# Performance work log

Measured on AMD Instinct MI355X. Metric: run time of the kernel, lower is better.

Reference implementation:

```python
import jax, jax.numpy as jnp
import numpy as np

B, S, H = 8, 2048, 1024

def setup_inputs() -> dict:
    key = jax.random.key(0)
    k1, k2 = jax.random.split(key)
    inputs = jax.random.normal(k1, (B, S, H), dtype=jnp.float32)
    # PyTorch Linear weight [out, in]; init ~ U(-1/sqrt(H), 1/sqrt(H)) approximated with scaled normal
    W = jax.random.normal(k2, (H, H), dtype=jnp.float32) * (1.0 / np.sqrt(H))
    b = jnp.zeros((H,), dtype=jnp.float32)
    return {"inputs": inputs, "W": W, "b": b}

def reference(inputs, W, b):
    # QW = inputs @ W^T + b   (nn.Linear)
    QW = jnp.einsum('bsh,oh->bso', inputs, W) + b  # [B,S,H]
    # score = QW @ inputs^T  (no scaling, no mask)
    score = jnp.einsum('bqh,bkh->bqk', QW, inputs)  # [B,S,S]
    attn = jax.nn.softmax(score, axis=2)
    # output = attn @ inputs
    output = jnp.einsum('bqk,bkh->bqh', attn, inputs)  # [B,S,H]
    return output
```

## Files before the change

### kernel.cpp

```cpp
#include <hip/hip_runtime.h>
#include <hip/hip_bf16.h>
#include <hip/hip_fp16.h>

typedef unsigned short u16;
typedef __attribute__((ext_vector_type(8))) _Float16 f16x8;
typedef __attribute__((ext_vector_type(4))) float f32x4;

#define B_ 8
#define S_ 2048
#define H_ 1024
#define M_ (B_ * S_)

__device__ __forceinline__ u16 f2h(float f) {
  _Float16 h = (_Float16)f;
  return __builtin_bit_cast(u16, h);
}

__global__ void f32_to_f16_kernel(const float* __restrict__ x,
                                  u16* __restrict__ o, int n4) {
  int stride = gridDim.x * blockDim.x;
  for (int i = blockIdx.x * blockDim.x + threadIdx.x; i < n4; i += stride) {
    float4 v = reinterpret_cast<const float4*>(x)[i];
    ushort4 h;
    h.x = f2h(v.x); h.y = f2h(v.y); h.z = f2h(v.z); h.w = f2h(v.w);
    reinterpret_cast<ushort4*>(o)[i] = h;
  }
}

__global__ void transpose_f32_kernel(const float* __restrict__ x,
                                     u16* __restrict__ xt,
                                     u16* __restrict__ xf) {
  __shared__ u16 t[64][65];
  int b = blockIdx.z, s0 = blockIdx.x * 64, h0 = blockIdx.y * 64;
  int tx = threadIdx.x, ty = threadIdx.y;
  const float* src = x + ((size_t)b * S_ + s0) * H_ + h0;
  u16* dstf = xf + ((size_t)b * S_ + s0) * H_ + h0;
#pragma unroll
  for (int i = 0; i < 4; ++i) {
    u16 h = f2h(src[(size_t)(ty + 16 * i) * H_ + tx]);
    t[ty + 16 * i][tx] = h;
    dstf[(size_t)(ty + 16 * i) * H_ + tx] = h;
  }
  __syncthreads();
  u16* dst = xt + ((size_t)b * H_ + h0) * S_ + s0;
#pragma unroll
  for (int i = 0; i < 4; ++i)
    dst[(size_t)(ty + 16 * i) * S_ + tx] = t[tx][ty + 16 * i];
}

__device__ __forceinline__ void async_stage16(const u16* g, u16* l) {
  __builtin_amdgcn_global_load_lds(
      (__attribute__((address_space(1))) void*)g,
      (__attribute__((address_space(3))) void*)l, 16, 0, 0);
}

template <int OM>
__global__ __launch_bounds__(512) void gemm8_kernel(
    const u16* __restrict__ A, const u16* __restrict__ B,
    float* __restrict__ Cf, u16* __restrict__ Ch,
    const float* __restrict__ bias,
    int lda, int ldb, int ldc, int K,
    long sAz, long sBz, long sCz) {
  __shared__ __align__(16) u16 sA[2][256 * 64];
  __shared__ __align__(16) u16 sB[2][256 * 64];

  int gx = gridDim.x, gy = gridDim.y;
  int nwg = gx * gy * gridDim.z;
  int wgid = blockIdx.x + gx * (blockIdx.y + gy * blockIdx.z);
  int q = nwg >> 3, r = nwg & 7;
  int xcd = wgid & 7, idx = wgid >> 3;
  int nid = (xcd < r ? xcd * (q + 1) : r * (q + 1) + (xcd - r) * q) + idx;
  int bxi = nid % gx, t2 = nid / gx;
  int byi = t2 % gy, bzi = t2 / gy;

  int tid = threadIdx.x, wave = tid >> 6, lane = tid & 63;
  int wm = wave >> 2, wn = wave & 3;
  int bm = bxi * 256, bn = byi * 256;
  long zA = (long)bzi * sAz;
  long zB = (long)bzi * sBz;
  long zC = (long)bzi * sCz;
  const u16* gA = A + zA + (size_t)bm * lda;
  const u16* gB = B + zB + (size_t)bn * ldb;

  int srow = tid >> 3;
  int scolb = (tid & 7) << 4;
  int sco = (scolb ^ ((srow & 7) << 4)) >> 1;
  size_t aO0 = (size_t)srow * lda + sco, aO1 = aO0 + (size_t)64 * lda;
  size_t bO0 = (size_t)srow * ldb + sco, bO1 = bO0 + (size_t)64 * ldb;
  int ld0 = srow * 64 + (scolb >> 1), ld1 = ld0 + 64 * 64;

  auto stgA = [&](int slot, int half, int kofs) {
    const u16* g = gA + (size_t)(half * 128) * lda + kofs;
    u16* l = &sA[slot][half * 8192];
    async_stage16(g + aO0, l + ld0);
    async_stage16(g + aO1, l + ld1);
  };
  auto stgB = [&](int slot, int half, int kofs) {
    const u16* g = gB + (size_t)(half * 128) * ldb + kofs;
    u16* l = &sB[slot][half * 8192];
    async_stage16(g + bO0, l + ld0);
    async_stage16(g + bO1, l + ld1);
  };

  int la = lane & 15;
  int kg = (lane >> 4) << 4;
  auto frag = [&](const u16* base, int row, int colb) -> f16x8 {
    int off = (row << 7) + (colb ^ ((row & 7) << 4));
    return *reinterpret_cast<const f16x8*>(
        reinterpret_cast<const char*>(base) + off);
  };

  f16x8 aF[4][2], bF[2][2];
  f32x4 acc[8][4] = {};

  auto RA = [&](int slot, int qm) {
#pragma unroll
    for (int j = 0; j < 4; ++j)
#pragma unroll
      for (int ks = 0; ks < 2; ++ks)
        aF[j][ks] = frag(sA[slot], qm * 128 + (j * 2 + wm) * 16 + la,
                         ks * 64 + kg);
  };
  auto RB = [&](int slot, int qn) {
#pragma unroll
    for (int i = 0; i < 2; ++i)
#pragma unroll
      for (int ks = 0; ks < 2; ++ks)
        bF[i][ks] = frag(sB[slot], qn * 128 + (i * 4 + wn) * 16 + la,
                         ks * 64 + kg);
  };
  auto MM = [&](int qm, int qn) {
#pragma unroll
    for (int ks = 0; ks < 2; ++ks)
#pragma unroll
      for (int j = 0; j < 4; ++j)
#pragma unroll
        for (int i = 0; i < 2; ++i)
          acc[qm * 4 + j][qn * 2 + i] = __builtin_amdgcn_mfma_f32_16x16x32_f16(
              aF[j][ks], bF[i][ks], acc[qm * 4 + j][qn * 2 + i], 0, 0, 0);
  };

#define VM6 asm volatile("s_waitcnt vmcnt(6)" ::: "memory")
#define VM0 asm volatile("s_waitcnt vmcnt(0)" ::: "memory")
#define LG8 asm volatile("s_waitcnt lgkmcnt(8)" ::: "memory")
#define BAR __builtin_amdgcn_s_barrier()
#define LG0                                              \
  asm volatile("s_waitcnt lgkmcnt(0)" ::: "memory");     \
  __builtin_amdgcn_sched_barrier(0)
#define MFMA_CL(qm, qn)                 \
  __builtin_amdgcn_s_setprio(1);        \
  MM(qm, qn);                           \
  __builtin_amdgcn_s_setprio(0)

  int NT = K >> 6;
  stgA(0, 0, 0); stgB(0, 0, 0); stgB(0, 1, 0); stgA(0, 1, 0);
  if (NT > 1) { stgA(1, 0, 64); stgB(1, 1, 64); stgA(1, 1, 64); }
  VM6;
  BAR;

  for (int t = 0; t < NT; ++t) {
    int s = t & 1, ns = s ^ 1;
    int k1 = (t + 1) << 6, k2 = (t + 2) << 6;
    bool p1 = (t + 1 < NT), p2 = (t + 2 < NT);
    RA(s, 0); RB(s, 0);
    if (p1) stgB(ns, 0, k1);
    LG8;
    BAR; LG0; MFMA_CL(0, 0); BAR;
    RB(s, 1);
    if (p2) stgA(s, 0, k2);
    BAR; LG0; MFMA_CL(0, 1); BAR;
    RA(s, 1);
    if (p2) stgB(s, 1, k2);
    BAR; LG0; MFMA_CL(1, 1); BAR;
    RB(s, 0);
    if (p2) stgA(s, 1, k2);
    if (t < NT - 2) { VM6; } else if (t == NT - 2) { VM0; }
    BAR; LG0; MFMA_CL(1, 0); BAR;
  }
#undef VM6
#undef VM0
#undef LG8
#undef BAR
#undef LG0
#undef MFMA_CL

#pragma unroll
  for (int mf = 0; mf < 8; ++mf) {
    int qm = mf >> 2, j = mf & 3;
    int row = bm + qm * 128 + (j * 2 + wm) * 16 + (lane >> 4) * 4;
#pragma unroll
    for (int nf = 0; nf < 4; ++nf) {
      int qn = nf >> 1, i = nf & 1;
      int col = bn + qn * 128 + (i * 4 + wn) * 16 + la;
#pragma unroll
      for (int r = 0; r < 4; ++r) {
        float v = acc[mf][nf][r];
        if constexpr (OM == 1) {
          Ch[zC + (size_t)(row + r) * ldc + col] = f2h(v + bias[col]);
        } else {
          Cf[zC + (size_t)(row + r) * ldc + col] = v;
        }
      }
    }
  }
}

__global__ __launch_bounds__(256) void softmax_kernel(const float* __restrict__ sc,
                                                      u16* __restrict__ attn,
                                                      int opitch) {
  __shared__ float red[4];
  size_t row = blockIdx.x;
  const float* p = sc + row * S_;
  u16* o = attn + row * (size_t)opitch;
  int t = threadIdx.x;
  float4 v0 = reinterpret_cast<const float4*>(p)[t];
  float4 v1 = reinterpret_cast<const float4*>(p)[t + 256];
  float mx = fmaxf(fmaxf(fmaxf(v0.x, v0.y), fmaxf(v0.z, v0.w)),
                   fmaxf(fmaxf(v1.x, v1.y), fmaxf(v1.z, v1.w)));
#pragma unroll
  for (int d = 32; d > 0; d >>= 1) mx = fmaxf(mx, __shfl_xor(mx, d));
  if ((t & 63) == 0) red[t >> 6] = mx;
  __syncthreads();
  mx = fmaxf(fmaxf(red[0], red[1]), fmaxf(red[2], red[3]));
  float e[8];
  e[0] = __expf(v0.x - mx); e[1] = __expf(v0.y - mx);
  e[2] = __expf(v0.z - mx); e[3] = __expf(v0.w - mx);
  e[4] = __expf(v1.x - mx); e[5] = __expf(v1.y - mx);
  e[6] = __expf(v1.z - mx); e[7] = __expf(v1.w - mx);
  float s = ((e[0] + e[1]) + (e[2] + e[3])) + ((e[4] + e[5]) + (e[6] + e[7]));
#pragma unroll
  for (int d = 32; d > 0; d >>= 1) s += __shfl_xor(s, d);
  __syncthreads();
  if ((t & 63) == 0) red[t >> 6] = s;
  __syncthreads();
  s = (red[0] + red[1]) + (red[2] + red[3]);
  float inv = 1.0f / s;
  ushort4 h0, h1;
  h0.x = f2h(e[0] * inv); h0.y = f2h(e[1] * inv);
  h0.z = f2h(e[2] * inv); h0.w = f2h(e[3] * inv);
  h1.x = f2h(e[4] * inv); h1.y = f2h(e[5] * inv);
  h1.z = f2h(e[6] * inv); h1.w = f2h(e[7] * inv);
  reinterpret_cast<ushort4*>(o)[t] = h0;
  reinterpret_cast<ushort4*>(o)[t + 256] = h1;
}

extern "C" void kernel_launch(void* const* d_in, const int* in_sizes, int n_in,
                              void* d_out, int out_size, void* d_ws, size_t ws_size,
                              hipStream_t stream) {
  const float* X = (const float*)d_in[0];
  const float* W = (const float*)d_in[1];
  const float* bias = (const float*)d_in[2];
  float* out = (float*)d_out;
  char* ws = (char*)d_ws;

  const size_t MB = 1ull << 20;
  u16* XF = (u16*)(ws);
  u16* WF = (u16*)(ws + 32 * MB);
  u16* XT = (u16*)(ws + 34 * MB);
  u16* QW = (u16*)(ws + 66 * MB);
  float* SC = (float*)(ws + 98 * MB);
  u16* PF = (u16*)(ws + 162 * MB);

  int plan = (ws_size >= 226 * MB) ? 2 : (ws_size >= 163 * MB) ? 1 : 0;
  int CB = (plan >= 1) ? 4 : 2;
  int nch = B_ / CB;

  f32_to_f16_kernel<<<1024, 256, 0, stream>>>(W, WF, H_ * H_ / 4);
  transpose_f32_kernel<<<dim3(S_ / 64, H_ / 64, B_), dim3(64, 16), 0, stream>>>(
      X, XT, XF);
  gemm8_kernel<1><<<dim3(M_ / 256, H_ / 256, 1), 512, 0, stream>>>(
      XF, WF, nullptr, QW, bias, H_, H_, H_, H_, 0, 0, 0);
  for (int ch = 0; ch < nch; ++ch) {
    long off = (long)ch * CB;
    gemm8_kernel<0><<<dim3(S_ / 256, S_ / 256, CB), 512, 0, stream>>>(
        QW + off * S_ * H_, XF + off * S_ * H_, SC, nullptr, nullptr,
        H_, H_, S_, H_, (long)S_ * H_, (long)S_ * H_, (long)S_ * S_);
    if (plan == 2) {
      softmax_kernel<<<CB * S_, 256, 0, stream>>>(
          SC, PF + off * S_ * S_, S_);
    } else {
      softmax_kernel<<<CB * S_, 256, 0, stream>>>(
          SC, (u16*)SC, 2 * S_);
      gemm8_kernel<0><<<dim3(S_ / 256, H_ / 256, CB), 512, 0, stream>>>(
          (u16*)SC, XT + off * (long)H_ * S_,
          out + off * (long)S_ * H_, nullptr, nullptr,
          2 * S_, S_, H_, S_, (long)S_ * 2 * S_, (long)H_ * S_, (long)S_ * H_);
    }
  }
  if (plan == 2) {
    gemm8_kernel<0><<<dim3(S_ / 256, H_ / 256, B_), 512, 0, stream>>>(
        PF, XT, out, nullptr, nullptr,
        S_, S_, H_, S_, (long)S_ * S_, (long)H_ * S_, (long)S_ * H_);
  }
}
```

Before: 257.3 us.

## Keep both B fragment halves in registers, drop redundant barriers, vectorize transpose

The GEMM main loop now holds the B fragments for both N-halves in separate registers. The last quadrant can then reuse the B fragments loaded earlier instead of reloading them from LDS, and several of the paired barriers around each MFMA cluster are removed to cut synchronisation stalls. The transpose/convert kernel switches to float4 loads and ushort4 stores with 256 threads and a padded LDS tile, which should make global accesses wider. The gemm changes raise register pressure, and fewer barriers could expose LDS write-after-read hazards if the staging order is not actually safe.

```diff
diff --git a/kernel.cpp b/kernel.cpp
--- a/kernel.cpp
+++ b/kernel.cpp
@@ -27,25 +27,34 @@
   }
 }
 
-__global__ void transpose_f32_kernel(const float* __restrict__ x,
-                                     u16* __restrict__ xt,
-                                     u16* __restrict__ xf) {
-  __shared__ u16 t[64][65];
+__global__ __launch_bounds__(256) void transpose_f32_kernel(
+    const float* __restrict__ x, u16* __restrict__ xt, u16* __restrict__ xf) {
+  __shared__ u16 t[64][72];
   int b = blockIdx.z, s0 = blockIdx.x * 64, h0 = blockIdx.y * 64;
-  int tx = threadIdx.x, ty = threadIdx.y;
-  const float* src = x + ((size_t)b * S_ + s0) * H_ + h0;
-  u16* dstf = xf + ((size_t)b * S_ + s0) * H_ + h0;
-#pragma unroll
-  for (int i = 0; i < 4; ++i) {
-    u16 h = f2h(src[(size_t)(ty + 16 * i) * H_ + tx]);
-    t[ty + 16 * i][tx] = h;
-    dstf[(size_t)(ty + 16 * i) * H_ + tx] = h;
+  int tid = threadIdx.x;
+  int row = tid & 63, seg = tid >> 6;
+  const float* src = x + ((size_t)(b * S_ + s0 + row)) * H_ + h0 + seg * 16;
+  u16* dstf = xf + ((size_t)(b * S_ + s0 + row)) * H_ + h0 + seg * 16;
+#pragma unroll
+  for (int j = 0; j < 4; ++j) {
+    float4 v = reinterpret_cast<const float4*>(src)[j];
+    ushort4 h;
+    h.x = f2h(v.x); h.y = f2h(v.y); h.z = f2h(v.z); h.w = f2h(v.w);
+    reinterpret_cast<ushort4*>(dstf)[j] = h;
+    *reinterpret_cast<ushort4*>(&t[row][seg * 16 + j * 4]) = h;
   }
   __syncthreads();
-  u16* dst = xt + ((size_t)b * H_ + h0) * S_ + s0;
-#pragma unroll
-  for (int i = 0; i < 4; ++i)
-    dst[(size_t)(ty + 16 * i) * S_ + tx] = t[tx][ty + 16 * i];
+  int hh = tid & 63, ss = tid >> 6;
+  u16* dst = xt + ((size_t)(b * H_ + h0 + hh)) * S_ + s0 + ss * 16;
+#pragma unroll
+  for (int j = 0; j < 4; ++j) {
+    ushort4 o;
+    o.x = t[ss * 16 + j * 4 + 0][hh];
+    o.y = t[ss * 16 + j * 4 + 1][hh];
+    o.z = t[ss * 16 + j * 4 + 2][hh];
+    o.w = t[ss * 16 + j * 4 + 3][hh];
+    reinterpret_cast<ushort4*>(dst)[j] = o;
+  }
 }
 
 __device__ __forceinline__ void async_stage16(const u16* g, u16* l) {
@@ -110,7 +119,8 @@
         reinterpret_cast<const char*>(base) + off);
   };
 
-  f16x8 aF[4][2], bF[2][2];
+  f16x8 aF[4][2];
+  f16x8 bF[2][2][2];
   f32x4 acc[8][4] = {};
 
   auto RA = [&](int slot, int qm) {
@@ -126,8 +136,8 @@
     for (int i = 0; i < 2; ++i)
 #pragma unroll
       for (int ks = 0; ks < 2; ++ks)
-        bF[i][ks] = frag(sB[slot], qn * 128 + (i * 4 + wn) * 16 + la,
-                         ks * 64 + kg);
+        bF[qn][i][ks] = frag(sB[slot], qn * 128 + (i * 4 + wn) * 16 + la,
+                             ks * 64 + kg);
   };
   auto MM = [&](int qm, int qn) {
 #pragma unroll
@@ -137,12 +147,11 @@
 #pragma unroll
         for (int i = 0; i < 2; ++i)
           acc[qm * 4 + j][qn * 2 + i] = __builtin_amdgcn_mfma_f32_16x16x32_f16(
-              aF[j][ks], bF[i][ks], acc[qm * 4 + j][qn * 2 + i], 0, 0, 0);
+              aF[j][ks], bF[qn][i][ks], acc[qm * 4 + j][qn * 2 + i], 0, 0, 0);
   };
 
 #define VM6 asm volatile("s_waitcnt vmcnt(6)" ::: "memory")
 #define VM0 asm volatile("s_waitcnt vmcnt(0)" ::: "memory")
-#define LG8 asm volatile("s_waitcnt lgkmcnt(8)" ::: "memory")
 #define BAR __builtin_amdgcn_s_barrier()
 #define LG0                                              \
   asm volatile("s_waitcnt lgkmcnt(0)" ::: "memory");     \
@@ -164,22 +173,20 @@
     bool p1 = (t + 1 < NT), p2 = (t + 2 < NT);
     RA(s, 0); RB(s, 0);
     if (p1) stgB(ns, 0, k1);
-    LG8;
-    BAR; LG0; MFMA_CL(0, 0); BAR;
+    LG0; MFMA_CL(0, 0); BAR;
     RB(s, 1);
     if (p2) stgA(s, 0, k2);
-    BAR; LG0; MFMA_CL(0, 1); BAR;
+    LG0; MFMA_CL(0, 1); BAR;
     RA(s, 1);
     if (p2) stgB(s, 1, k2);
-    BAR; LG0; MFMA_CL(1, 1); BAR;
-    RB(s, 0);
+    LG0; MFMA_CL(1, 1); BAR;
     if (p2) stgA(s, 1, k2);
+    MFMA_CL(1, 0);
     if (t < NT - 2) { VM6; } else if (t == NT - 2) { VM0; }
-    BAR; LG0; MFMA_CL(1, 0); BAR;
+    BAR;
   }
 #undef VM6
 #undef VM0
-#undef LG8
 #undef BAR
 #undef LG0
 #undef MFMA_CL
@@ -266,7 +273,7 @@
   int nch = B_ / CB;
 
   f32_to_f16_kernel<<<1024, 256, 0, stream>>>(W, WF, H_ * H_ / 4);
-  transpose_f32_kernel<<<dim3(S_ / 64, H_ / 64, B_), dim3(64, 16), 0, stream>>>(
+  transpose_f32_kernel<<<dim3(S_ / 64, H_ / 64, B_), 256, 0, stream>>>(
       X, XT, XF);
   gemm8_kernel<1><<<dim3(M_ / 256, H_ / 256, 1), 512, 0, stream>>>(
       XF, WF, nullptr, QW, bias, H_, H_, H_, H_, 0, 0, 0);
```

Measured after the change: 263.7 us. +2.5%, slower.
